# Performance work log

Measured on AMD Instinct MI355X. Metric: run time of the kernel, lower is better.

## Reference

```python
import jax, jax.numpy as jnp
import numpy as np

N, E = 100000, 3200000
IN, HID, OUT, ED = 16, 64, 32, 3
BN_EPS = 1e-5


def setup_inputs() -> dict:
    key = jax.random.key(0)
    ks = jax.random.split(key, 40)
    d = {}
    d["x"] = jax.random.normal(ks[0], (N, IN), jnp.float32)
    d["edge_index"] = jax.random.randint(ks[1], (2, E), 0, N, dtype=jnp.int32)
    d["edge_attr"] = jax.random.normal(ks[2], (E, ED), jnp.float32)
    i = [3]
    def p(shape):
        w = jax.random.normal(ks[i[0]], shape, jnp.float32) * 0.05
        i[0] += 1
        return w
    for tag, nd in (("inj1", IN), ("inj2", HID), ("inj3", HID)):
        d[tag + "_w1"] = p((ED, nd)); d[tag + "_b1"] = p((nd,))
        d[tag + "_w2"] = p((nd, nd)); d[tag + "_b2"] = p((nd,))
    for tag, ci, co in (("conv1", IN, HID), ("conv2", HID, HID), ("conv3", HID, OUT)):
        d[tag + "_wl"] = p((ci, co)); d[tag + "_bl"] = p((co,))
        d[tag + "_wr"] = p((ci, co))
    for tag, c in (("bn1", HID), ("bn2", HID), ("bn3", OUT)):
        d[tag + "_w"] = p((c,)); d[tag + "_b"] = p((c,))
    return d


def _inject(x, src, dst, edge_attr, w1, b1, w2, b2):
    # edge MLP: [E, ED] -> [E, node_dim], sigmoid wind gate from column 2
    h = jax.nn.relu(edge_attr @ w1 + b1) @ w2 + b2
    gate = jax.nn.sigmoid(edge_attr[:, 2:3])
    msg = h * gate
    agg = jax.ops.segment_sum(msg, dst, num_segments=x.shape[0])
    return x + agg


def _sage(x, src, dst, wl, bl, wr):
    # PyG SAGEConv (mean aggr): lin_l(mean_{j in N(i)} x_j) + lin_r(x_i)
    n = x.shape[0]
    s = jax.ops.segment_sum(x[src], dst, num_segments=n)
    cnt = jax.ops.segment_sum(jnp.ones((src.shape[0], 1), x.dtype), dst, num_segments=n)
    mean = s / jnp.maximum(cnt, 1.0)
    return mean @ wl + bl + x @ wr


def _bn(x, w, b):
    # eval-mode BatchNorm with running_mean=0, running_var=1
    return x * (w / jnp.sqrt(1.0 + BN_EPS)) + b


def reference(x, edge_index, edge_attr,
              inj1_w1, inj1_b1, inj1_w2, inj1_b2,
              inj2_w1, inj2_b1, inj2_w2, inj2_b2,
              inj3_w1, inj3_b1, inj3_w2, inj3_b2,
              conv1_wl, conv1_bl, conv1_wr,
              conv2_wl, conv2_bl, conv2_wr,
              conv3_wl, conv3_bl, conv3_wr,
              bn1_w, bn1_b, bn2_w, bn2_b, bn3_w, bn3_b):
    src, dst = edge_index[0], edge_index[1]
    h = _inject(x, src, dst, edge_attr, inj1_w1, inj1_b1, inj1_w2, inj1_b2)
    h = jax.nn.relu(_bn(_sage(h, src, dst, conv1_wl, conv1_bl, conv1_wr), bn1_w, bn1_b))
    h = _inject(h, src, dst, edge_attr, inj2_w1, inj2_b1, inj2_w2, inj2_b2)
    h = jax.nn.relu(_bn(_sage(h, src, dst, conv2_wl, conv2_bl, conv2_wr), bn2_w, bn2_b))
    h = _inject(h, src, dst, edge_attr, inj3_w1, inj3_b1, inj3_w2, inj3_b2)
    h = jax.nn.relu(_bn(_sage(h, src, dst, conv3_wl, conv3_bl, conv3_wr), bn3_w, bn3_b))
    return h
```

## Files before the change

kernel.cpp:

```cpp
#include <hip/hip_runtime.h>
#include <math.h>

#define N_NODES 100000
#define N_EDGES 3200000
#define NB 391
#define CHUNK 4096
#define NCHUNK 782
#define HCHUNK 4096
#define NHCHUNK 782
#define CAPB 10240

constexpr size_t al512(size_t x){ return (x + 511) & ~size_t(511); }
constexpr size_t o_bcnt = 0;
constexpr size_t o_bst  = al512(o_bcnt + 512*4);
constexpr size_t o_gb   = al512(o_bst  + 512*4);
constexpr size_t o_off  = al512(o_gb   + 512*4);
constexpr size_t o_srcp = al512(o_off  + ((size_t)N_NODES+1)*4);
constexpr size_t o_epk  = al512(o_srcp + (size_t)N_EDGES*4);
constexpr size_t o_U1   = al512(o_epk  + (size_t)N_EDGES*16);
constexpr size_t o_U2   = al512(o_U1   + (size_t)N_NODES*16*4);
constexpr size_t o_U3   = o_U2 + (size_t)N_NODES*64*4;
constexpr size_t o_gs   = al512(o_U3   + (size_t)N_NODES*64*4);
constexpr size_t o_h1   = al512(o_gs   + (size_t)N_NODES*4);
constexpr size_t o_m1   = al512(o_h1   + (size_t)N_NODES*16*4);
constexpr size_t o_rec  = o_U2;
constexpr size_t o_h2bf = o_epk;
constexpr size_t o_h3bf = o_epk + (size_t)N_NODES*128;
constexpr size_t o_m2   = o_U2;
constexpr size_t o_y3   = o_U1;
constexpr size_t o_m3p  = o_U2;

#define BN_RSQRT 0.9999950000374997f

__device__ __forceinline__ float4 ld4(const float* p){ return *(const float4*)p; }
__device__ __forceinline__ float fc(const float4& v, int i){ return ((const float*)&v)[i]; }
__device__ __forceinline__ float uf(unsigned u){ return __uint_as_float(u); }

__device__ __forceinline__ unsigned f2bf(float x){
    unsigned u = __float_as_uint(x);
    u += 0x7fffu + ((u >> 16) & 1u);
    return u >> 16;
}

__global__ __launch_bounds__(256) void khistBin(const int* __restrict__ dst,
                                                int* __restrict__ binCnt){
    __shared__ int c[NB];
    int t = threadIdx.x;
    for(int i=t; i<NB; i+=256) c[i] = 0;
    __syncthreads();
    long base = (long)blockIdx.x*HCHUNK;
    int nrem = (int)(N_EDGES - base); if(nrem > HCHUNK) nrem = HCHUNK;
    for(int k=t; k<nrem; k+=256)
        atomicAdd(&c[dst[base+k] >> 8], 1);
    __syncthreads();
    for(int i=t; i<NB; i+=256)
        if(c[i]) atomicAdd(&binCnt[i], c[i]);
}

__global__ __launch_bounds__(512) void kscanBin(const int* __restrict__ binCnt,
                                                int* __restrict__ binStart,
                                                int* __restrict__ gbase){
    __shared__ int s[512];
    int t = threadIdx.x;
    int v = (t < NB) ? binCnt[t] : 0;
    s[t] = v; __syncthreads();
    for(int off=1; off<512; off<<=1){
        int a = (t>=off) ? s[t-off] : 0;
        __syncthreads(); s[t] += a; __syncthreads();
    }
    int ex = (t==0) ? 0 : s[t-1];
    if(t < NB){ binStart[t] = ex; gbase[t] = ex; }
    if(t == NB) binStart[NB] = s[NB-1];
}

__global__ __launch_bounds__(256) void kbinA(const int* __restrict__ src,
                                             const int* __restrict__ dst,
                                             const float* __restrict__ ea,
                                             int* __restrict__ gbase,
                                             unsigned* __restrict__ recD){
    __shared__ int cnt[NB], lofs[NB], gst[NB], lcnt[NB];
    __shared__ int sscan[256];
    __shared__ unsigned stage[CHUNK*3];
    __shared__ unsigned short binOf[CHUNK];
    int t = threadIdx.x;
    long e0i = (long)blockIdx.x*CHUNK;
    int nrem = (int)(N_EDGES - e0i); if(nrem > CHUNK) nrem = CHUNK;
    if(nrem <= 0) return;

    for(int b=t; b<NB; b+=256){ cnt[b]=0; lcnt[b]=0; }
    __syncthreads();
    for(int k=t; k<nrem; k+=256)
        atomicAdd(&cnt[dst[e0i+k] >> 8], 1);
    __syncthreads();
    int c0 = (2*t   < NB) ? cnt[2*t]   : 0;
    int c1 = (2*t+1 < NB) ? cnt[2*t+1] : 0;
    sscan[t] = c0 + c1;
    __syncthreads();
    for(int off=1; off<256; off<<=1){
        int v = (t>=off) ? sscan[t-off] : 0;
        __syncthreads(); sscan[t] += v; __syncthreads();
    }
    int base = (t==0) ? 0 : sscan[t-1];
    if(2*t   < NB) lofs[2*t]   = base;
    if(2*t+1 < NB) lofs[2*t+1] = base + c0;
    for(int b=t; b<NB; b+=256){
        int c = cnt[b];
        gst[b] = c ? atomicAdd(&gbase[b], c) : 0;
    }
    __syncthreads();
    for(int k=t; k<nrem; k+=256){
        long i = e0i + k;
        int d = dst[i];
        int s = src[i];
        float a0 = ea[i*3+0], a1 = ea[i*3+1], a2 = ea[i*3+2];
        int b = d >> 8;
        int p = lofs[b] + atomicAdd(&lcnt[b], 1);
        stage[3*p+0] = (unsigned)s | ((unsigned)(d & 255) << 17);
        stage[3*p+1] = (f2bf(a1)<<16) | f2bf(a0);
        stage[3*p+2] = __float_as_uint(a2);
        binOf[p] = (unsigned short)b;
    }
    __syncthreads();
    int total3 = nrem*3;
    for(int q=t; q<total3; q+=256){
        int p = q/3;
        int r = q - 3*p;
        int b = binOf[p];
        int g = gst[b] + (p - lofs[b]);
        recD[(size_t)3*g + r] = stage[q];
    }
}

__global__ __launch_bounds__(512) void kbinB(const unsigned* __restrict__ recD,
                                             const int* __restrict__ binStart,
                                             int* __restrict__ offs,
                                             int* __restrict__ srcp,
                                             float4* __restrict__ epk){
    __shared__ int pfx[257], lcnt[256];
    __shared__ int sscan[256];
    __shared__ unsigned short perm[CAPB];
    __shared__ unsigned char  nibOf[CAPB];
    int t = threadIdx.x;
    int b = blockIdx.x;
    int n0 = b*256;
    int nn = N_NODES - n0; if(nn > 256) nn = 256;
    int base = binStart[b];
    int m    = binStart[b+1] - base;
    for(int i=t; i<256; i+=512) lcnt[i] = 0;
    __syncthreads();
    for(int p=t; p<m; p+=512){
        unsigned w0 = recD[(size_t)3*(base+p)];
        int nib = (int)((w0 >> 17) & 255u);
        if(p < CAPB) nibOf[p] = (unsigned char)nib;
        atomicAdd(&lcnt[nib], 1);
    }
    __syncthreads();
    if(t < 256) sscan[t] = lcnt[t];
    __syncthreads();
    if(t < 256){
        for(int off=1; off<256; off<<=1){
            int v = (t>=off) ? sscan[t-off] : 0;
            __syncthreads(); sscan[t] += v; __syncthreads();
        }
        pfx[t+1] = sscan[t];
        if(t==0) pfx[0] = 0;
    } else {
        for(int off=1; off<256; off<<=1){ __syncthreads(); __syncthreads(); }
    }
    __syncthreads();
    for(int i=t; i<=nn; i+=512) offs[n0+i] = base + pfx[i];
    for(int i=t; i<256; i+=512) lcnt[i] = 0;
    __syncthreads();
    for(int p=t; p<m; p+=512){
        int nib = nibOf[p];
        int slot = pfx[nib] + atomicAdd(&lcnt[nib], 1);
        perm[slot] = (unsigned short)p;
    }
    __syncthreads();
    for(int s=t; s<m; s+=512){
        size_t q = (size_t)3*(base + (int)perm[s]);
        unsigned w0 = recD[q], w1 = recD[q+1], w2 = recD[q+2];
        float e2 = uf(w2);
        float gate = __builtin_amdgcn_rcpf(1.f + __expf(-e2));
        srcp[base+s] = (int)(w0 & 0x1FFFFu);
        epk [base+s] = make_float4(uf(w1<<16), uf(w1 & 0xffff0000u), e2, gate);
    }
}

#define EDGE_ACC(r) { \
    float h_ = fmaf((r).z,wc1, fmaf((r).y,wb1, fmaf((r).x,wa1, bb1))); \
    a1 = fmaf(fmaxf(h_,0.f), (r).w, a1); \
    _Pragma("unroll") \
    for(int k_=0;k_<4;k_++){ \
        float h2_ = fmaf((r).z,wc2[k_], fmaf((r).y,wb2[k_], fmaf((r).x,wa2[k_], bv2[k_]))); \
        a2[k_] = fmaf(fmaxf(h2_,0.f), (r).w, a2[k_]); \
        float h3_ = fmaf((r).z,wc3[k_], fmaf((r).y,wb3[k_], fmaf((r).x,wa3[k_], bv3[k_]))); \
        a3[k_] = fmaf(fmaxf(h3_,0.f), (r).w, a3[k_]); \
    } \
    g += (r).w; }

__global__ __launch_bounds__(256,4) void kinject(const float4* __restrict__ epk, const int* __restrict__ offs,
                        const float* __restrict__ w11, const float* __restrict__ b11,
                        const float* __restrict__ w12, const float* __restrict__ b12,
                        const float* __restrict__ w13, const float* __restrict__ b13,
                        float* __restrict__ U1, float* __restrict__ U2,
                        float* __restrict__ U3, float* __restrict__ gsum){
    int gid = blockIdx.x*blockDim.x + threadIdx.x;
    int node = gid >> 6;
    if(node >= N_NODES) return;
    int lane = threadIdx.x & 63;
    int q = lane >> 4, j = lane & 15;
    float wa1=w11[j], wb1=w11[16+j], wc1=w11[32+j], bb1=b11[j];
    float wa2[4], wb2[4], wc2[4], bv2[4], wa3[4], wb3[4], wc3[4], bv3[4];
    #pragma unroll
    for(int k=0;k<4;k++){
        int c = j + 16*k;
        wa2[k]=w12[c]; wb2[k]=w12[64+c]; wc2[k]=w12[128+c]; bv2[k]=b12[c];
        wa3[k]=w13[c]; wb3[k]=w13[64+c]; wc3[k]=w13[128+c]; bv3[k]=b13[c];
    }
    int beg = offs[node], end = offs[node+1];
    float a1=0.f, g=0.f;
    float a2[4] = {0.f,0.f,0.f,0.f};
    float a3[4] = {0.f,0.f,0.f,0.f};
    int e = beg;
    int efull = beg + ((end - beg) & ~7);
    for(; e < efull; e+=8){
        float4 r0 = epk[e + q];
        float4 r1 = epk[e + 4 + q];
        EDGE_ACC(r0);
        EDGE_ACC(r1);
    }
    if(e < end){
        int ee0 = e + q, ee1 = e + 4 + q;
        float4 r0 = (ee0 < end) ? epk[ee0] : make_float4(0.f,0.f,0.f,0.f);
        float4 r1 = (ee1 < end) ? epk[ee1] : make_float4(0.f,0.f,0.f,0.f);
        EDGE_ACC(r0);
        EDGE_ACC(r1);
    }
    #pragma unroll
    for(int k=0;k<4;k++){
        a2[k] += __shfl_xor(a2[k], 16); a2[k] += __shfl_xor(a2[k], 32);
        a3[k] += __shfl_xor(a3[k], 16); a3[k] += __shfl_xor(a3[k], 32);
    }
    a1 += __shfl_xor(a1, 16); a1 += __shfl_xor(a1, 32);
    g  += __shfl_xor(g, 16);  g  += __shfl_xor(g, 32);
    float v2 = (q==0) ? a2[0] : (q==1) ? a2[1] : (q==2) ? a2[2] : a2[3];
    float v3 = (q==0) ? a3[0] : (q==1) ? a3[1] : (q==2) ? a3[2] : a3[3];
    U2[(size_t)node*64 + lane] = v2;
    U3[(size_t)node*64 + lane] = v3;
    if(lane < 16) U1[node*16 + j] = a1;
    if(lane == 0) gsum[node] = g;
}

__global__ void kgather16(const float* __restrict__ h, const int* __restrict__ srcp,
                          const int* __restrict__ offs, float* __restrict__ m){
    int gid = blockIdx.x*blockDim.x + threadIdx.x;
    int node = gid >> 6;
    if(node >= N_NODES) return;
    int lane = threadIdx.x & 63;
    int q = lane >> 4, d = lane & 15;
    int beg = offs[node], end = offs[node+1];
    float acc = 0.f;
    for(int e=beg+q; e<end; e+=4) acc += h[(size_t)srcp[e]*16 + d];
    acc += __shfl_down(acc, 32);
    acc += __shfl_down(acc, 16);
    if(lane < 16){
        float c = fmaxf((float)(end-beg), 1.f);
        m[node*16 + lane] = acc / c;
    }
}

__global__ void kgather64bf(const unsigned* __restrict__ hbf, const int* __restrict__ srcp,
                            const int* __restrict__ offs, float* __restrict__ m){
    int gid = blockIdx.x*blockDim.x + threadIdx.x;
    int node = gid >> 6;
    if(node >= N_NODES) return;
    int lane = threadIdx.x & 63;
    int q = lane >> 4, j = lane & 15;
    int beg = offs[node], end = offs[node+1];
    float4 acc = make_float4(0.f,0.f,0.f,0.f);
    int e = beg;
    int efull = beg + ((end - beg) & ~7);
    for(; e < efull; e+=8){
        int s0 = srcp[e + q], s1 = srcp[e + 4 + q];
        uint2 w0 = *(const uint2*)(hbf + (size_t)s0*32 + 2*j);
        uint2 w1 = *(const uint2*)(hbf + (size_t)s1*32 + 2*j);
        acc.x += uf(w0.x<<16); acc.y += uf(w0.x & 0xffff0000u);
        acc.z += uf(w0.y<<16); acc.w += uf(w0.y & 0xffff0000u);
        acc.x += uf(w1.x<<16); acc.y += uf(w1.x & 0xffff0000u);
        acc.z += uf(w1.y<<16); acc.w += uf(w1.y & 0xffff0000u);
    }
    for(; e < end; e+=4){
        int ee = e + q;
        if(ee < end){
            int s = srcp[ee];
            uint2 w = *(const uint2*)(hbf + (size_t)s*32 + 2*j);
            acc.x += uf(w.x<<16); acc.y += uf(w.x & 0xffff0000u);
            acc.z += uf(w.y<<16); acc.w += uf(w.y & 0xffff0000u);
        }
    }
    acc.x += __shfl_xor(acc.x,16); acc.x += __shfl_xor(acc.x,32);
    acc.y += __shfl_xor(acc.y,16); acc.y += __shfl_xor(acc.y,32);
    acc.z += __shfl_xor(acc.z,16); acc.z += __shfl_xor(acc.z,32);
    acc.w += __shfl_xor(acc.w,16); acc.w += __shfl_xor(acc.w,32);
    if(lane < 16){
        float inv = 1.f / fmaxf((float)(end-beg), 1.f);
        float4 o; o.x=acc.x*inv; o.y=acc.y*inv; o.z=acc.z*inv; o.w=acc.w*inv;
        *(float4*)(m + (size_t)node*64 + 4*j) = o;
    }
}

__global__ void kgather32bf(const unsigned* __restrict__ y3, const int* __restrict__ srcp,
                            const int* __restrict__ offs, float* __restrict__ m){
    int gid = blockIdx.x*blockDim.x + threadIdx.x;
    int node = gid >> 6;
    if(node >= N_NODES) return;
    int lane = threadIdx.x & 63;
    int q = lane >> 4, j = lane & 15;
    int beg = offs[node], end = offs[node+1];
    float ax=0.f, ay=0.f;
    int e = beg;
    int efull = beg + ((end - beg) & ~7);
    for(; e < efull; e+=8){
        unsigned w0 = y3[(size_t)srcp[e + q]*16 + j];
        unsigned w1 = y3[(size_t)srcp[e + 4 + q]*16 + j];
        ax += uf(w0<<16); ay += uf(w0 & 0xffff0000u);
        ax += uf(w1<<16); ay += uf(w1 & 0xffff0000u);
    }
    for(; e < end; e+=4){
        int ee = e + q;
        if(ee < end){
            unsigned w = y3[(size_t)srcp[ee]*16 + j];
            ax += uf(w<<16); ay += uf(w & 0xffff0000u);
        }
    }
    ax += __shfl_xor(ax,16); ax += __shfl_xor(ax,32);
    ay += __shfl_xor(ay,16); ay += __shfl_xor(ay,32);
    if(lane < 16){
        float inv = 1.f / fmaxf((float)(end-beg), 1.f);
        float2 o; o.x = ax*inv; o.y = ay*inv;
        *(float2*)(m + (size_t)node*32 + 2*j) = o;
    }
}


__global__ __launch_bounds__(256) void kdense0(const float* __restrict__ x, const float* __restrict__ U1,
                        const float* __restrict__ gs, const float* __restrict__ w2,
                        const float* __restrict__ b2, float* __restrict__ h1){
    __shared__ float sw[256];
    int t = threadIdx.x;
    sw[t] = w2[t];
    __syncthreads();
    int idx = blockIdx.x*256 + t;
    int n = idx >> 4, j = idx & 15;
    float acc = x[idx] + gs[n]*b2[j];
    const float4* row = (const float4*)(U1 + n*16);
    #pragma unroll
    for(int i4=0;i4<4;i4++){
        float4 r = row[i4];
        acc += r.x*sw[(i4*4+0)*16 + j];
        acc += r.y*sw[(i4*4+1)*16 + j];
        acc += r.z*sw[(i4*4+2)*16 + j];
        acc += r.w*sw[(i4*4+3)*16 + j];
    }
    h1[idx] = acc;
}

__global__ __launch_bounds__(256) void kdense1(const float* __restrict__ m1, const float* __restrict__ h1,
                        const float* __restrict__ U2, const float* __restrict__ gs,
                        const float* __restrict__ wl, const float* __restrict__ bl,
                        const float* __restrict__ wr,
                        const float* __restrict__ w2, const float* __restrict__ b2,
                        const float* __restrict__ bnw, const float* __restrict__ bnb,
                        unsigned* __restrict__ h2bf){
    __shared__ float4 swl[16*16];
    __shared__ float4 swr[16*16];
    __shared__ float4 sw2[64*16];
    int t = threadIdx.x;
    swl[t] = ((const float4*)wl)[t];
    swr[t] = ((const float4*)wr)[t];
    #pragma unroll
    for(int k=0;k<4;k++) sw2[t + 256*k] = ((const float4*)w2)[t + 256*k];
    __syncthreads();

    int w = t>>6, l = t&63;
    int jg = l&15, j0 = jg*4, ng = l>>4;
    int nb = blockIdx.x*64 + w*16 + ng*4;
    int nn[4];
    #pragma unroll
    for(int k=0;k<4;k++) nn[k] = (nb+k < N_NODES) ? nb+k : N_NODES-1;

    float a[4][4], b[4][4];
    float4 blv = ld4(bl + j0);
    float4 b2v = ld4(b2 + j0);
    #pragma unroll
    for(int k=0;k<4;k++){
        float g = gs[nn[k]];
        a[k][0]=blv.x; a[k][1]=blv.y; a[k][2]=blv.z; a[k][3]=blv.w;
        b[k][0]=g*b2v.x; b[k][1]=g*b2v.y; b[k][2]=g*b2v.z; b[k][3]=g*b2v.w;
    }
    #pragma unroll
    for(int i=0;i<16;i+=4){
        float4 rm[4], rh[4];
        #pragma unroll
        for(int k=0;k<4;k++){ rm[k] = ld4(m1 + nn[k]*16 + i); rh[k] = ld4(h1 + nn[k]*16 + i); }
        #pragma unroll
        for(int ii=0;ii<4;ii++){
            float4 wL = swl[(i+ii)*16 + jg];
            float4 wR = swr[(i+ii)*16 + jg];
            #pragma unroll
            for(int k=0;k<4;k++){
                float vm = fc(rm[k],ii), vh = fc(rh[k],ii);
                a[k][0] = fmaf(vm,wL.x, fmaf(vh,wR.x, a[k][0]));
                a[k][1] = fmaf(vm,wL.y, fmaf(vh,wR.y, a[k][1]));
                a[k][2] = fmaf(vm,wL.z, fmaf(vh,wR.z, a[k][2]));
                a[k][3] = fmaf(vm,wL.w, fmaf(vh,wR.w, a[k][3]));
            }
        }
    }
    #pragma unroll 4
    for(int i=0;i<64;i+=4){
        float4 ru[4];
        #pragma unroll
        for(int k=0;k<4;k++) ru[k] = ld4(U2 + (size_t)nn[k]*64 + i);
        #pragma unroll
        for(int ii=0;ii<4;ii++){
            float4 wv = sw2[(i+ii)*16 + jg];
            #pragma unroll
            for(int k=0;k<4;k++){
                float vu = fc(ru[k],ii);
                b[k][0] = fmaf(vu,wv.x,b[k][0]);
                b[k][1] = fmaf(vu,wv.y,b[k][1]);
                b[k][2] = fmaf(vu,wv.z,b[k][2]);
                b[k][3] = fmaf(vu,wv.w,b[k][3]);
            }
        }
    }
    float4 bw = ld4(bnw + j0), bb = ld4(bnb + j0);
    #pragma unroll
    for(int k=0;k<4;k++){
        if(nb+k < N_NODES){
            float ox = fmaxf(a[k][0]*(bw.x*BN_RSQRT)+bb.x,0.f) + b[k][0];
            float oy = fmaxf(a[k][1]*(bw.y*BN_RSQRT)+bb.y,0.f) + b[k][1];
            float oz = fmaxf(a[k][2]*(bw.z*BN_RSQRT)+bb.z,0.f) + b[k][2];
            float ow = fmaxf(a[k][3]*(bw.w*BN_RSQRT)+bb.w,0.f) + b[k][3];
            uint2 pk; pk.x = f2bf(ox) | (f2bf(oy)<<16); pk.y = f2bf(oz) | (f2bf(ow)<<16);
            *(uint2*)(h2bf + (size_t)(nb+k)*32 + (j0>>1)) = pk;
        }
    }
}

__global__ __launch_bounds__(256) void kdense2(const float* __restrict__ m2, const unsigned* __restrict__ h2bf,
                        const float* __restrict__ U3, const float* __restrict__ gs,
                        const float* __restrict__ wl, const float* __restrict__ bl,
                        const float* __restrict__ wr,
                        const float* __restrict__ w2, const float* __restrict__ b2,
                        const float* __restrict__ bnw, const float* __restrict__ bnb,
                        const float* __restrict__ wl3,
                        unsigned* __restrict__ h3bf, unsigned* __restrict__ y3){
    __shared__ float4 swl[64*16];
    __shared__ float4 swr[64*16];
    __shared__ float4 sw2[64*16];
    __shared__ float4 swl3[64*8];
    __shared__ unsigned sh3[64*32];
    int t = threadIdx.x;
    #pragma unroll
    for(int k=0;k<4;k++){
        swl[t + 256*k] = ((const float4*)wl)[t + 256*k];
        swr[t + 256*k] = ((const float4*)wr)[t + 256*k];
        sw2[t + 256*k] = ((const float4*)w2)[t + 256*k];
    }
    swl3[t] = ((const float4*)wl3)[t];
    swl3[t+256] = ((const float4*)wl3)[t+256];
    __syncthreads();

    int w = t>>6, l = t&63;
    int jg = l&15, j0 = jg*4, ng = l>>4;
    int ln0 = w*16 + ng*4;
    int nb = blockIdx.x*64 + ln0;
    int nn[4];
    #pragma unroll
    for(int k=0;k<4;k++) nn[k] = (nb+k < N_NODES) ? nb+k : N_NODES-1;

    float a[4][4], b[4][4];
    float4 blv = ld4(bl + j0);
    float4 b2v = ld4(b2 + j0);
    #pragma unroll
    for(int k=0;k<4;k++){
        float g = gs[nn[k]];
        a[k][0]=blv.x; a[k][1]=blv.y; a[k][2]=blv.z; a[k][3]=blv.w;
        b[k][0]=g*b2v.x; b[k][1]=g*b2v.y; b[k][2]=g*b2v.z; b[k][3]=g*b2v.w;
    }
    #pragma unroll 4
    for(int i=0;i<64;i+=4){
        float4 rm[4], rh[4];
        #pragma unroll
        for(int k=0;k<4;k++){
            rm[k] = ld4(m2 + (size_t)nn[k]*64 + i);
            uint2 hw = *(const uint2*)(h2bf + (size_t)nn[k]*32 + (i>>1));
            rh[k].x = uf(hw.x<<16); rh[k].y = uf(hw.x & 0xffff0000u);
            rh[k].z = uf(hw.y<<16); rh[k].w = uf(hw.y & 0xffff0000u);
        }
        #pragma unroll
        for(int ii=0;ii<4;ii++){
            float4 wL = swl[(i+ii)*16 + jg];
            float4 wR = swr[(i+ii)*16 + jg];
            #pragma unroll
            for(int k=0;k<4;k++){
                float vm = fc(rm[k],ii), vh = fc(rh[k],ii);
                a[k][0] = fmaf(vm,wL.x, fmaf(vh,wR.x, a[k][0]));
                a[k][1] = fmaf(vm,wL.y, fmaf(vh,wR.y, a[k][1]));
                a[k][2] = fmaf(vm,wL.z, fmaf(vh,wR.z, a[k][2]));
                a[k][3] = fmaf(vm,wL.w, fmaf(vh,wR.w, a[k][3]));
            }
        }
    }
    #pragma unroll 4
    for(int i=0;i<64;i+=4){
        float4 ru[4];
        #pragma unroll
        for(int k=0;k<4;k++) ru[k] = ld4(U3 + (size_t)nn[k]*64 + i);
        #pragma unroll
        for(int ii=0;ii<4;ii++){
            float4 wv = sw2[(i+ii)*16 + jg];
            #pragma unroll
            for(int k=0;k<4;k++){
                float vu = fc(ru[k],ii);
                b[k][0] = fmaf(vu,wv.x,b[k][0]);
                b[k][1] = fmaf(vu,wv.y,b[k][1]);
                b[k][2] = fmaf(vu,wv.z,b[k][2]);
                b[k][3] = fmaf(vu,wv.w,b[k][3]);
            }
        }
    }
    float4 bw = ld4(bnw + j0), bb = ld4(bnb + j0);
    #pragma unroll
    for(int k=0;k<4;k++){
        float ox = fmaxf(a[k][0]*(bw.x*BN_RSQRT)+bb.x,0.f) + b[k][0];
        float oy = fmaxf(a[k][1]*(bw.y*BN_RSQRT)+bb.y,0.f) + b[k][1];
        float oz = fmaxf(a[k][2]*(bw.z*BN_RSQRT)+bb.z,0.f) + b[k][2];
        float ow = fmaxf(a[k][3]*(bw.w*BN_RSQRT)+bb.w,0.f) + b[k][3];
        uint2 pk; pk.x = f2bf(ox) | (f2bf(oy)<<16); pk.y = f2bf(oz) | (f2bf(ow)<<16);
        *(uint2*)(sh3 + (ln0+k)*32 + (j0>>1)) = pk;
        if(nb+k < N_NODES)
            *(uint2*)(h3bf + (size_t)(nb+k)*32 + (j0>>1)) = pk;
    }
    __syncthreads();
    int nl = t >> 2, jc = t & 3;
    int gnode = blockIdx.x*64 + nl;
    if(gnode < N_NODES){
        float y[8] = {0.f,0.f,0.f,0.f,0.f,0.f,0.f,0.f};
        #pragma unroll 8
        for(int i2=0; i2<32; ++i2){
            unsigned hw = sh3[nl*32 + i2];
            float h0 = uf(hw<<16), h1 = uf(hw & 0xffff0000u);
            float4 A0 = swl3[(2*i2)*8 + jc*2];
            float4 A1 = swl3[(2*i2)*8 + jc*2 + 1];
            float4 B0 = swl3[(2*i2+1)*8 + jc*2];
            float4 B1 = swl3[(2*i2+1)*8 + jc*2 + 1];
            y[0] = fmaf(h0,A0.x, fmaf(h1,B0.x, y[0]));
            y[1] = fmaf(h0,A0.y, fmaf(h1,B0.y, y[1]));
            y[2] = fmaf(h0,A0.z, fmaf(h1,B0.z, y[2]));
            y[3] = fmaf(h0,A0.w, fmaf(h1,B0.w, y[3]));
            y[4] = fmaf(h0,A1.x, fmaf(h1,B1.x, y[4]));
            y[5] = fmaf(h0,A1.y, fmaf(h1,B1.y, y[5]));
            y[6] = fmaf(h0,A1.z, fmaf(h1,B1.z, y[6]));
            y[7] = fmaf(h0,A1.w, fmaf(h1,B1.w, y[7]));
        }
        uint4 pk;
        pk.x = f2bf(y[0]) | (f2bf(y[1])<<16);
        pk.y = f2bf(y[2]) | (f2bf(y[3])<<16);
        pk.z = f2bf(y[4]) | (f2bf(y[5])<<16);
        pk.w = f2bf(y[6]) | (f2bf(y[7])<<16);
        *(uint4*)(y3 + (size_t)gnode*16 + jc*4) = pk;
    }
}

__global__ __launch_bounds__(256) void kdense3(const float* __restrict__ m3p, const unsigned* __restrict__ h3bf,
                        const float* __restrict__ bl,
                        const float* __restrict__ wr,
                        const float* __restrict__ bnw, const float* __restrict__ bnb,
                        float* __restrict__ out){
    __shared__ float4 swr[64*8];
    int t = threadIdx.x;
    #pragma unroll
    for(int k=0;k<2;k++) swr[t + 256*k] = ((const float4*)wr)[t + 256*k];
    __syncthreads();

    int w = t>>6, l = t&63;
    int jg = l&7, j0 = jg*4, ng = l>>3;
    int nb = blockIdx.x*128 + w*32 + ng*4;
    int nn[4];
    #pragma unroll
    for(int k=0;k<4;k++) nn[k] = (nb+k < N_NODES) ? nb+k : N_NODES-1;

    float a[4][4];
    float4 blv = ld4(bl + j0);
    #pragma unroll
    for(int k=0;k<4;k++){
        float4 mp = ld4(m3p + (size_t)nn[k]*32 + j0);
        a[k][0]=blv.x+mp.x; a[k][1]=blv.y+mp.y; a[k][2]=blv.z+mp.z; a[k][3]=blv.w+mp.w;
    }
    #pragma unroll 4
    for(int i=0;i<64;i+=4){
        float4 rh[4];
        #pragma unroll
        for(int k=0;k<4;k++){
            uint2 hw = *(const uint2*)(h3bf + (size_t)nn[k]*32 + (i>>1));
            rh[k].x = uf(hw.x<<16); rh[k].y = uf(hw.x & 0xffff0000u);
            rh[k].z = uf(hw.y<<16); rh[k].w = uf(hw.y & 0xffff0000u);
        }
        #pragma unroll
        for(int ii=0;ii<4;ii++){
            float4 wR = swr[(i+ii)*8 + jg];
            #pragma unroll
            for(int k=0;k<4;k++){
                float vh = fc(rh[k],ii);
                a[k][0] = fmaf(vh,wR.x,a[k][0]);
                a[k][1] = fmaf(vh,wR.y,a[k][1]);
                a[k][2] = fmaf(vh,wR.z,a[k][2]);
                a[k][3] = fmaf(vh,wR.w,a[k][3]);
            }
        }
    }
    float4 bw = ld4(bnw + j0), bb = ld4(bnb + j0);
    #pragma unroll
    for(int k=0;k<4;k++){
        if(nb+k < N_NODES){
            float4 o;
            o.x = fmaxf(a[k][0]*(bw.x*BN_RSQRT)+bb.x,0.f);
            o.y = fmaxf(a[k][1]*(bw.y*BN_RSQRT)+bb.y,0.f);
            o.z = fmaxf(a[k][2]*(bw.z*BN_RSQRT)+bb.z,0.f);
            o.w = fmaxf(a[k][3]*(bw.w*BN_RSQRT)+bb.w,0.f);
            *(float4*)(out + (size_t)(nb+k)*32 + j0) = o;
        }
    }
}

extern "C" void kernel_launch(void* const* d_in, const int* in_sizes, int n_in,
                              void* d_out, int out_size, void* d_ws, size_t ws_size,
                              hipStream_t stream){
    const float* x    = (const float*)d_in[0];
    const int*   ei   = (const int*)  d_in[1];
    const float* ea   = (const float*)d_in[2];
    const float* i1w1 = (const float*)d_in[3];
    const float* i1b1 = (const float*)d_in[4];
    const float* i1w2 = (const float*)d_in[5];
    const float* i1b2 = (const float*)d_in[6];
    const float* i2w1 = (const float*)d_in[7];
    const float* i2b1 = (const float*)d_in[8];
    const float* i2w2 = (const float*)d_in[9];
    const float* i2b2 = (const float*)d_in[10];
    const float* i3w1 = (const float*)d_in[11];
    const float* i3b1 = (const float*)d_in[12];
    const float* i3w2 = (const float*)d_in[13];
    const float* i3b2 = (const float*)d_in[14];
    const float* c1wl = (const float*)d_in[15];
    const float* c1bl = (const float*)d_in[16];
    const float* c1wr = (const float*)d_in[17];
    const float* c2wl = (const float*)d_in[18];
    const float* c2bl = (const float*)d_in[19];
    const float* c2wr = (const float*)d_in[20];
    const float* c3wl = (const float*)d_in[21];
    const float* c3bl = (const float*)d_in[22];
    const float* c3wr = (const float*)d_in[23];
    const float* bn1w = (const float*)d_in[24];
    const float* bn1b = (const float*)d_in[25];
    const float* bn2w = (const float*)d_in[26];
    const float* bn2b = (const float*)d_in[27];
    const float* bn3w = (const float*)d_in[28];
    const float* bn3b = (const float*)d_in[29];

    char* ws = (char*)d_ws;
    int*      bcnt = (int*)     (ws + o_bcnt);
    int*      bst  = (int*)     (ws + o_bst);
    int*      gb   = (int*)     (ws + o_gb);
    int*      offs = (int*)     (ws + o_off);
    int*      srcp = (int*)     (ws + o_srcp);
    float4*   epk  = (float4*)  (ws + o_epk);
    unsigned* recD = (unsigned*)(ws + o_rec);
    float*    U1   = (float*)   (ws + o_U1);
    float*    U2   = (float*)   (ws + o_U2);
    float*    U3   = (float*)   (ws + o_U3);
    float*    gs   = (float*)   (ws + o_gs);
    float*    h1   = (float*)   (ws + o_h1);
    float*    m1   = (float*)   (ws + o_m1);
    unsigned* h2bf = (unsigned*)(ws + o_h2bf);
    unsigned* h3bf = (unsigned*)(ws + o_h3bf);
    float*    m2   = (float*)   (ws + o_m2);
    unsigned* y3   = (unsigned*)(ws + o_y3);
    float*    m3p  = (float*)   (ws + o_m3p);

    const int* src = ei;
    const int* dst = ei + N_EDGES;

    hipMemsetAsync(bcnt, 0, 512*4, stream);
    khistBin <<<NHCHUNK, 256, 0, stream>>>(dst, bcnt);
    kscanBin <<<1,       512, 0, stream>>>(bcnt, bst, gb);
    kbinA  <<<NCHUNK, 256, 0, stream>>>(src, dst, ea, gb, recD);
    kbinB  <<<NB,     512, 0, stream>>>(recD, bst, offs, srcp, epk);

    kinject <<<N_NODES/4, 256, 0, stream>>>(epk, offs,
                                            i1w1, i1b1, i2w1, i2b1, i3w1, i3b1,
                                            U1, U2, U3, gs);
    kdense0 <<<N_NODES*16/256, 256, 0, stream>>>(x, U1, gs, i1w2, i1b2, h1);
    kgather16<<<N_NODES/4, 256, 0, stream>>>(h1, srcp, offs, m1);
    kdense1 <<<(N_NODES+63)/64, 256, 0, stream>>>(m1, h1, U2, gs,
                                                 c1wl, c1bl, c1wr, i2w2, i2b2,
                                                 bn1w, bn1b, h2bf);
    kgather64bf<<<N_NODES/4, 256, 0, stream>>>(h2bf, srcp, offs, m2);
    kdense2 <<<(N_NODES+63)/64, 256, 0, stream>>>(m2, h2bf, U3, gs,
                                                 c2wl, c2bl, c2wr, i3w2, i3b2,
                                                 bn2w, bn2b, c3wl, h3bf, y3);
    kgather32bf<<<N_NODES/4, 256, 0, stream>>>(y3, srcp, offs, m3p);
    kdense3 <<<(N_NODES+127)/128, 256, 0, stream>>>(m3p, h3bf, c3bl, c3wr,
                                                 bn3w, bn3b, (float*)d_out);
}
```

Before: 685.6 us.

## Remap injection edge-MLP kernel to 2 edges per step, 8 nodes per wave

Restructures the fused edge-MLP injection kernel so each wave handles 8 consecutive nodes and each lane covers 2 columns of the 64-wide hidden layers. Each step now processes 2 edges instead of 4, instead of every lane computing 4 columns per edge. This cuts the redundant per-edge MLP work across lanes, since each edge's hidden units are computed by fewer lanes. It also amortises the weight loads across nodes and drops the 4-wave occupancy hint. The cost is fewer edges in flight per load and a serial loop over nodes within a wave, which may worsen load imbalance and latency hiding.

```diff
diff --git a/kernel.cpp b/kernel.cpp
--- a/kernel.cpp
+++ b/kernel.cpp
@@ -9,6 +9,9 @@
 #define HCHUNK 4096
 #define NHCHUNK 782
 #define CAPB 10240
+#define NPW 8
+#define NWAVES ((N_NODES + NPW - 1)/NPW)
+#define NBLK_INJ ((NWAVES + 3)/4)
 
 constexpr size_t al512(size_t x){ return (x + 511) & ~size_t(511); }
 constexpr size_t o_bcnt = 0;
@@ -187,69 +190,67 @@
     }
 }
 
-#define EDGE_ACC(r) { \
-    float h_ = fmaf((r).z,wc1, fmaf((r).y,wb1, fmaf((r).x,wa1, bb1))); \
-    a1 = fmaf(fmaxf(h_,0.f), (r).w, a1); \
-    _Pragma("unroll") \
-    for(int k_=0;k_<4;k_++){ \
-        float h2_ = fmaf((r).z,wc2[k_], fmaf((r).y,wb2[k_], fmaf((r).x,wa2[k_], bv2[k_]))); \
-        a2[k_] = fmaf(fmaxf(h2_,0.f), (r).w, a2[k_]); \
-        float h3_ = fmaf((r).z,wc3[k_], fmaf((r).y,wb3[k_], fmaf((r).x,wa3[k_], bv3[k_]))); \
-        a3[k_] = fmaf(fmaxf(h3_,0.f), (r).w, a3[k_]); \
-    } \
+#define ACC2(r) { \
+    float h1_ = fmaf((r).z,wc1, fmaf((r).y,wb1, fmaf((r).x,wa1, bb1))); \
+    a1 = fmaf(fmaxf(h1_,0.f), (r).w, a1); \
+    float h2a_ = fmaf((r).z,wc2a, fmaf((r).y,wb2a, fmaf((r).x,wa2a, bv2a))); \
+    a2a = fmaf(fmaxf(h2a_,0.f), (r).w, a2a); \
+    float h2b_ = fmaf((r).z,wc2b, fmaf((r).y,wb2b, fmaf((r).x,wa2b, bv2b))); \
+    a2b = fmaf(fmaxf(h2b_,0.f), (r).w, a2b); \
+    float h3a_ = fmaf((r).z,wc3a, fmaf((r).y,wb3a, fmaf((r).x,wa3a, bv3a))); \
+    a3a = fmaf(fmaxf(h3a_,0.f), (r).w, a3a); \
+    float h3b_ = fmaf((r).z,wc3b, fmaf((r).y,wb3b, fmaf((r).x,wa3b, bv3b))); \
+    a3b = fmaf(fmaxf(h3b_,0.f), (r).w, a3b); \
     g += (r).w; }
 
-__global__ __launch_bounds__(256,4) void kinject(const float4* __restrict__ epk, const int* __restrict__ offs,
+__global__ __launch_bounds__(256) void kinject(const float4* __restrict__ epk, const int* __restrict__ offs,
                         const float* __restrict__ w11, const float* __restrict__ b11,
                         const float* __restrict__ w12, const float* __restrict__ b12,
                         const float* __restrict__ w13, const float* __restrict__ b13,
                         float* __restrict__ U1, float* __restrict__ U2,
                         float* __restrict__ U3, float* __restrict__ gsum){
-    int gid = blockIdx.x*blockDim.x + threadIdx.x;
-    int node = gid >> 6;
-    if(node >= N_NODES) return;
+    int wid = (blockIdx.x*256 + threadIdx.x) >> 6;
+    int n0 = wid * NPW;
+    if(n0 >= N_NODES) return;
+    int n1 = n0 + NPW; if(n1 > N_NODES) n1 = N_NODES;
     int lane = threadIdx.x & 63;
-    int q = lane >> 4, j = lane & 15;
-    float wa1=w11[j], wb1=w11[16+j], wc1=w11[32+j], bb1=b11[j];
-    float wa2[4], wb2[4], wc2[4], bv2[4], wa3[4], wb3[4], wc3[4], bv3[4];
-    #pragma unroll
-    for(int k=0;k<4;k++){
-        int c = j + 16*k;
-        wa2[k]=w12[c]; wb2[k]=w12[64+c]; wc2[k]=w12[128+c]; bv2[k]=b12[c];
-        wa3[k]=w13[c]; wb3[k]=w13[64+c]; wc3[k]=w13[128+c]; bv3[k]=b13[c];
-    }
-    int beg = offs[node], end = offs[node+1];
-    float a1=0.f, g=0.f;
-    float a2[4] = {0.f,0.f,0.f,0.f};
-    float a3[4] = {0.f,0.f,0.f,0.f};
-    int e = beg;
-    int efull = beg + ((end - beg) & ~7);
-    for(; e < efull; e+=8){
-        float4 r0 = epk[e + q];
-        float4 r1 = epk[e + 4 + q];
-        EDGE_ACC(r0);
-        EDGE_ACC(r1);
-    }
-    if(e < end){
-        int ee0 = e + q, ee1 = e + 4 + q;
-        float4 r0 = (ee0 < end) ? epk[ee0] : make_float4(0.f,0.f,0.f,0.f);
-        float4 r1 = (ee1 < end) ? epk[ee1] : make_float4(0.f,0.f,0.f,0.f);
-        EDGE_ACC(r0);
-        EDGE_ACC(r1);
-    }
-    #pragma unroll
-    for(int k=0;k<4;k++){
-        a2[k] += __shfl_xor(a2[k], 16); a2[k] += __shfl_xor(a2[k], 32);
-        a3[k] += __shfl_xor(a3[k], 16); a3[k] += __shfl_xor(a3[k], 32);
-    }
-    a1 += __shfl_xor(a1, 16); a1 += __shfl_xor(a1, 32);
-    g  += __shfl_xor(g, 16);  g  += __shfl_xor(g, 32);
-    float v2 = (q==0) ? a2[0] : (q==1) ? a2[1] : (q==2) ? a2[2] : a2[3];
-    float v3 = (q==0) ? a3[0] : (q==1) ? a3[1] : (q==2) ? a3[2] : a3[3];
-    U2[(size_t)node*64 + lane] = v2;
-    U3[(size_t)node*64 + lane] = v3;
-    if(lane < 16) U1[node*16 + j] = a1;
-    if(lane == 0) gsum[node] = g;
+    int half = lane >> 5, j = lane & 31, j16 = lane & 15;
+    float wa1=w11[j16], wb1=w11[16+j16], wc1=w11[32+j16], bb1=b11[j16];
+    float wa2a=w12[j],    wb2a=w12[64+j],  wc2a=w12[128+j],  bv2a=b12[j];
+    float wa2b=w12[32+j], wb2b=w12[96+j],  wc2b=w12[160+j],  bv2b=b12[32+j];
+    float wa3a=w13[j],    wb3a=w13[64+j],  wc3a=w13[128+j],  bv3a=b13[j];
+    float wa3b=w13[32+j], wb3b=w13[96+j],  wc3b=w13[160+j],  bv3b=b13[32+j];
+
+    for(int node=n0; node<n1; ++node){
+        int beg = offs[node], end = offs[node+1];
+        float a1=0.f, a2a=0.f, a2b=0.f, a3a=0.f, a3b=0.f, g=0.f;
+        int e = beg;
+        int efull = beg + ((end - beg) & ~3);
+        for(; e < efull; e+=4){
+            float4 r0 = epk[e + half];
+            float4 r1 = epk[e + 2 + half];
+            ACC2(r0);
+            ACC2(r1);
+        }
+        if(e < end){
+            int ee0 = e + half, ee1 = e + 2 + half;
+            float4 r0 = (ee0 < end) ? epk[ee0] : make_float4(0.f,0.f,0.f,0.f);
+            float4 r1 = (ee1 < end) ? epk[ee1] : make_float4(0.f,0.f,0.f,0.f);
+            ACC2(r0);
+            ACC2(r1);
+        }
+        a2a += __shfl_xor(a2a, 32); a2b += __shfl_xor(a2b, 32);
+        a3a += __shfl_xor(a3a, 32); a3b += __shfl_xor(a3b, 32);
+        a1  += __shfl_xor(a1, 16);  a1  += __shfl_xor(a1, 32);
+        g   += __shfl_xor(g, 32);
+        float v2 = half ? a2b : a2a;
+        float v3 = half ? a3b : a3a;
+        int col = j + 32*half;
+        U2[(size_t)node*64 + col] = v2;
+        U3[(size_t)node*64 + col] = v3;
+        if(lane < 16) U1[node*16 + j16] = a1;
+        if(lane == 0) gsum[node] = g;
+    }
 }
 
 __global__ void kgather16(const float* __restrict__ h, const int* __restrict__ srcp,
@@ -700,9 +701,9 @@
     kbinA  <<<NCHUNK, 256, 0, stream>>>(src, dst, ea, gb, recD);
     kbinB  <<<NB,     512, 0, stream>>>(recD, bst, offs, srcp, epk);
 
-    kinject <<<N_NODES/4, 256, 0, stream>>>(epk, offs,
-                                            i1w1, i1b1, i2w1, i2b1, i3w1, i3b1,
-                                            U1, U2, U3, gs);
+    kinject <<<NBLK_INJ, 256, 0, stream>>>(epk, offs,
+                                           i1w1, i1b1, i2w1, i2b1, i3w1, i3b1,
+                                           U1, U2, U3, gs);
     kdense0 <<<N_NODES*16/256, 256, 0, stream>>>(x, U1, gs, i1w2, i1b2, h1);
     kgather16<<<N_NODES/4, 256, 0, stream>>>(h1, srcp, offs, m1);
     kdense1 <<<(N_NODES+63)/64, 256, 0, stream>>>(m1, h1, U2, gs,
```

Result: no change. 685.1 us (-0.1%).
